# Kernel tuning notes

Hardware: AMD Instinct MI355X
Metric: run time of the kernel (lower is better)

The kernel has to match this reference:

```python
import jax, jax.numpy as jnp
import numpy as np

B, S, D_MODEL, D_SPACE = 4, 2048, 1024, 64
N = 512            # size of each neuron pool (all six equal)
TOTAL = 6 * N      # neuron_emb rows
K = 8              # top_k for all four attention branches
EPS = 1e-8


def topk_sparsify(w, k):
    """Top-k sparsification with renormalization via dense one-hot scatter-sum.
    w: [..., N] softmax probs -> sparse renormalized [..., N]."""
    vals, idx = jax.lax.top_k(w, k)                       # [..., k]
    n = w.shape[-1]
    one_hot = jax.nn.one_hot(idx, n, dtype=w.dtype)       # [..., k, N]
    sparse = (one_hot * vals[..., None]).sum(axis=-2)     # [..., N]
    return sparse / (sparse.sum(axis=-1, keepdims=True) + EPS)


def setup_inputs() -> dict:
    key = jax.random.key(0)
    kx, kw, ke = jax.random.split(key, 3)
    x = jax.random.normal(kx, (B, S, D_MODEL), dtype=jnp.float32)
    W_all = jax.random.normal(kw, (D_MODEL, 6 * D_SPACE), dtype=jnp.float32) * 0.02
    b_all = jnp.zeros((6 * D_SPACE,), dtype=jnp.float32)
    neuron_emb = jax.random.normal(ke, (TOTAL, D_SPACE), dtype=jnp.float32) * 0.02
    return {"x": x, "W_all": W_all, "b_all": b_all, "neuron_emb": neuron_emb}


def reference(x, W_all, b_all, neuron_emb):
    # L2-normalized neuron embeddings (cosine-sim logits)
    emb = neuron_emb / (jnp.linalg.norm(neuron_emb, axis=-1, keepdims=True) + EPS)
    # dense projection, then split into 6 heads of d_space (deterministic: no dropout)
    proj = x @ W_all + b_all                              # [B,S,6*d_space]
    h = jnp.split(proj, 6, axis=-1)
    # neuron_emb segments: fqk, fv, rqk, rv (knowledge segments unused here)
    segs = [emb[0:N], emb[0:N], emb[N:2 * N], emb[2 * N:3 * N], emb[2 * N:3 * N], emb[3 * N:4 * N]]
    weights = []
    for hi, ei in zip(h, segs):
        logits = jnp.einsum('bsd,nd->bsn', hi, ei)        # [B,S,N]
        pref = jax.nn.softmax(logits, axis=-1)
        weights.append(topk_sparsify(pref, K))
    # [6, B, S, N]: (fqk_Q, fqk_K, fv, rqk_Q, rqk_K, rv)
    return jnp.stack(weights, axis=0)
```

## Files before the change

kernel.cpp:

```cpp
#include <hip/hip_runtime.h>
#include <math.h>

#define NB 4
#define NS 2048
#define DMODEL 1024
#define DSPACE 64
#define NPOOL 512
#define NHEADS 6
#define NTOK (NB * NS)
#define PROJN (NHEADS * DSPACE)
#define EPSF 1e-8f

typedef float f32x2 __attribute__((ext_vector_type(2)));

#define PK_LO(ACC, A2, B2) \
    asm("v_pk_fma_f32 %0, %1, %2, %0 op_sel:[0,0,0] op_sel_hi:[1,0,1]" \
        : "+v"(ACC) : "v"(A2), "v"(B2))
#define PK_HI(ACC, A2, B2) \
    asm("v_pk_fma_f32 %0, %1, %2, %0 op_sel:[0,1,0] op_sel_hi:[1,1,1]" \
        : "+v"(ACC) : "v"(A2), "v"(B2))

__global__ __launch_bounds__(256) void k_norm_emb(const float* __restrict__ emb,
                                                  float* __restrict__ embT) {
    int row  = blockIdx.x * 4 + (threadIdx.x >> 6);
    int lane = threadIdx.x & 63;
    float v  = emb[row * DSPACE + lane];
    float ss = v * v;
#pragma unroll
    for (int off = 32; off >= 1; off >>= 1) ss += __shfl_xor(ss, off, 64);
    float nrm = sqrtf(ss) + EPSF;
    embT[lane * 2048 + row] = v / nrm;
}

__global__ __launch_bounds__(128, 4) void k_proj(const float* __restrict__ X,
                                                 const float* __restrict__ W,
                                                 const float* __restrict__ bias,
                                                 float* __restrict__ P, int KS) {
    __shared__ float Xt[16 * 128];
    __shared__ float Wt[2][16 * 64];
    const int tid = threadIdx.x;
    const int w   = tid >> 6;
    const int L   = tid & 63;
    const int bm  = blockIdx.x * 128;
    const int bn  = blockIdx.y * 64;
    const int z   = blockIdx.z;
    float* Pp = P + (size_t)z * NTOK * PROJN;

    const int r0  = (tid >> 3) << 2;
    const int c0  = (tid & 7) << 2;
    const int xrow = w * 32 + (L & 31) + ((L & 32) << 1);
    const int wrr = L >> 2;
    const int wcc = (L & 3) << 4;

    const float* Xrow = X + (size_t)(bm + xrow) * DMODEL;
    float* wtp = &Wt[w][0];

    f32x2 acc2[4][8];
#pragma unroll
    for (int p = 0; p < 4; ++p)
#pragma unroll
        for (int j = 0; j < 8; ++j) acc2[p][j] = (f32x2){0.f, 0.f};

    const int nsteps = KS >> 4;
    int k0 = z * KS;
    float4 xr0 = *(const float4*)&Xrow[k0 + 0];
    float4 xr1 = *(const float4*)&Xrow[k0 + 4];
    float4 xr2 = *(const float4*)&Xrow[k0 + 8];
    float4 xr3 = *(const float4*)&Xrow[k0 + 12];
    float4 wa0 = *(const float4*)&W[(size_t)(k0 + wrr) * PROJN + bn + wcc + 0];
    float4 wa1 = *(const float4*)&W[(size_t)(k0 + wrr) * PROJN + bn + wcc + 4];
    float4 wa2 = *(const float4*)&W[(size_t)(k0 + wrr) * PROJN + bn + wcc + 8];
    float4 wa3 = *(const float4*)&W[(size_t)(k0 + wrr) * PROJN + bn + wcc + 12];

    {
        Xt[ 0*128+xrow]=xr0.x; Xt[ 1*128+xrow]=xr0.y; Xt[ 2*128+xrow]=xr0.z; Xt[ 3*128+xrow]=xr0.w;
        Xt[ 4*128+xrow]=xr1.x; Xt[ 5*128+xrow]=xr1.y; Xt[ 6*128+xrow]=xr1.z; Xt[ 7*128+xrow]=xr1.w;
        Xt[ 8*128+xrow]=xr2.x; Xt[ 9*128+xrow]=xr2.y; Xt[10*128+xrow]=xr2.z; Xt[11*128+xrow]=xr2.w;
        Xt[12*128+xrow]=xr3.x; Xt[13*128+xrow]=xr3.y; Xt[14*128+xrow]=xr3.z; Xt[15*128+xrow]=xr3.w;
        *(float4*)&wtp[wrr * 64 + wcc + 0]  = wa0;
        *(float4*)&wtp[wrr * 64 + wcc + 4]  = wa1;
        *(float4*)&wtp[wrr * 64 + wcc + 8]  = wa2;
        *(float4*)&wtp[wrr * 64 + wcc + 12] = wa3;
    }

    for (int s = 0; s < nsteps; ++s) {
        if (s + 1 < nsteps) {
            int k1 = k0 + 16;
            xr0 = *(const float4*)&Xrow[k1 + 0];
            xr1 = *(const float4*)&Xrow[k1 + 4];
            xr2 = *(const float4*)&Xrow[k1 + 8];
            xr3 = *(const float4*)&Xrow[k1 + 12];
            wa0 = *(const float4*)&W[(size_t)(k1 + wrr) * PROJN + bn + wcc + 0];
            wa1 = *(const float4*)&W[(size_t)(k1 + wrr) * PROJN + bn + wcc + 4];
            wa2 = *(const float4*)&W[(size_t)(k1 + wrr) * PROJN + bn + wcc + 8];
            wa3 = *(const float4*)&W[(size_t)(k1 + wrr) * PROJN + bn + wcc + 12];
        }
#pragma unroll
        for (int kk = 0; kk < 16; ++kk) {
            float4 a0 = *(const float4*)&Xt[kk * 128 + r0];
            float4 a1 = *(const float4*)&Xt[kk * 128 + r0 + 64];
            float4 b0 = *(const float4*)&wtp[kk * 64 + c0];
            float4 b1 = *(const float4*)&wtp[kk * 64 + c0 + 32];
            f32x2 ap0 = (f32x2){a0.x, a0.y};
            f32x2 ap1 = (f32x2){a0.z, a0.w};
            f32x2 ap2 = (f32x2){a1.x, a1.y};
            f32x2 ap3 = (f32x2){a1.z, a1.w};
            f32x2 bq0 = (f32x2){b0.x, b0.y};
            f32x2 bq1 = (f32x2){b0.z, b0.w};
            f32x2 bq2 = (f32x2){b1.x, b1.y};
            f32x2 bq3 = (f32x2){b1.z, b1.w};
#pragma unroll
            for (int p = 0; p < 4; ++p) {
                f32x2 ap = (p == 0) ? ap0 : (p == 1) ? ap1 : (p == 2) ? ap2 : ap3;
                PK_LO(acc2[p][0], ap, bq0); PK_HI(acc2[p][1], ap, bq0);
                PK_LO(acc2[p][2], ap, bq1); PK_HI(acc2[p][3], ap, bq1);
                PK_LO(acc2[p][4], ap, bq2); PK_HI(acc2[p][5], ap, bq2);
                PK_LO(acc2[p][6], ap, bq3); PK_HI(acc2[p][7], ap, bq3);
            }
        }
        if (s + 1 < nsteps) {
            Xt[ 0*128+xrow]=xr0.x; Xt[ 1*128+xrow]=xr0.y; Xt[ 2*128+xrow]=xr0.z; Xt[ 3*128+xrow]=xr0.w;
            Xt[ 4*128+xrow]=xr1.x; Xt[ 5*128+xrow]=xr1.y; Xt[ 6*128+xrow]=xr1.z; Xt[ 7*128+xrow]=xr1.w;
            Xt[ 8*128+xrow]=xr2.x; Xt[ 9*128+xrow]=xr2.y; Xt[10*128+xrow]=xr2.z; Xt[11*128+xrow]=xr2.w;
            Xt[12*128+xrow]=xr3.x; Xt[13*128+xrow]=xr3.y; Xt[14*128+xrow]=xr3.z; Xt[15*128+xrow]=xr3.w;
            *(float4*)&wtp[wrr * 64 + wcc + 0]  = wa0;
            *(float4*)&wtp[wrr * 64 + wcc + 4]  = wa1;
            *(float4*)&wtp[wrr * 64 + wcc + 8]  = wa2;
            *(float4*)&wtp[wrr * 64 + wcc + 12] = wa3;
        }
        k0 += 16;
    }

#pragma unroll
    for (int i = 0; i < 8; ++i) {
        int row = bm + r0 + ((i < 4) ? i : 60 + i);
        float o0[4], o1[4];
#pragma unroll
        for (int j = 0; j < 4; ++j) {
            f32x2 v0 = acc2[i >> 1][j];
            f32x2 v1 = acc2[i >> 1][j + 4];
            o0[j] = (i & 1) ? v0.y : v0.x;
            o1[j] = (i & 1) ? v1.y : v1.x;
        }
        if (z == 0) {
#pragma unroll
            for (int j = 0; j < 4; ++j) {
                o0[j] += bias[bn + c0 + j];
                o1[j] += bias[bn + c0 + 32 + j];
            }
        }
        *(float4*)&Pp[(size_t)row * PROJN + bn + c0]      = *(float4*)&o0[0];
        *(float4*)&Pp[(size_t)row * PROJN + bn + c0 + 32] = *(float4*)&o1[0];
    }
}

#define CE(arr, a, b) { float _hi = fmaxf(arr[a], arr[b]); arr[b] = fminf(arr[a], arr[b]); arr[a] = _hi; }

#define SORT8(s) \
    CE(s,0,1) CE(s,2,3) CE(s,4,5) CE(s,6,7) \
    CE(s,0,2) CE(s,1,3) CE(s,4,6) CE(s,5,7) \
    CE(s,1,2) CE(s,5,6) \
    CE(s,0,4) CE(s,1,5) CE(s,2,6) CE(s,3,7) \
    CE(s,2,4) CE(s,3,5) \
    CE(s,1,2) CE(s,3,4) CE(s,5,6)

#define SWZ(v, IMM) __int_as_float(__builtin_amdgcn_ds_swizzle(__float_as_int(v), IMM))

#define BFLY_LEVEL(XCHG) { \
    float q[4][8]; \
    _Pragma("unroll") \
    for (int tt = 0; tt < 4; ++tt) { \
        _Pragma("unroll") \
        for (int i = 0; i < 8; ++i) { float _x = s[tt][i]; q[tt][i] = XCHG(_x); } \
    } \
    _Pragma("unroll") \
    for (int tt = 0; tt < 4; ++tt) { \
        float c[8]; \
        c[0] = fmaxf(s[tt][0], q[tt][7]); c[1] = fmaxf(s[tt][1], q[tt][6]); \
        c[2] = fmaxf(s[tt][2], q[tt][5]); c[3] = fmaxf(s[tt][3], q[tt][4]); \
        c[4] = fmaxf(s[tt][4], q[tt][3]); c[5] = fmaxf(s[tt][5], q[tt][2]); \
        c[6] = fmaxf(s[tt][6], q[tt][1]); c[7] = fmaxf(s[tt][7], q[tt][0]); \
        CE(c,0,4) CE(c,1,5) CE(c,2,6) CE(c,3,7) \
        CE(c,0,2) CE(c,1,3) CE(c,4,6) CE(c,5,7) \
        CE(c,0,1) CE(c,2,3) CE(c,4,5) CE(c,6,7) \
        _Pragma("unroll") \
        for (int i = 0; i < 8; ++i) s[tt][i] = c[i]; \
    } }

#define X1(v)  SWZ(v, 0x041F)
#define X2(v)  SWZ(v, 0x081F)
#define X4(v)  SWZ(v, 0x101F)
#define X8(v)  SWZ(v, 0x201F)
#define X16(v) SWZ(v, 0x401F)
#define X32(v) __shfl_xor(v, 32, 64)

__global__ __launch_bounds__(256, 2) void k_router(const float* __restrict__ P,
                                                   const float* __restrict__ embT,
                                                   float* __restrict__ out, int SK) {
    __shared__ float hsh[32][DSPACE];
    const int head = blockIdx.y;
    const int t0   = blockIdx.x * 32;
    const int tid  = threadIdx.x;
    const int wid  = tid >> 6;
    const int lane = tid & 63;
    const int so = (head == 2) ? 512 : (head == 3 || head == 4) ? 1024
                 : (head == 5) ? 1536 : 0;

    {
        int t  = (wid << 3) + (lane >> 3);
        int d0 = (lane & 7) << 3;
        size_t off = (size_t)(t0 + t) * PROJN + head * DSPACE + d0;
        float4 v0 = *(const float4*)&P[off];
        float4 v1 = *(const float4*)&P[off + 4];
        for (int ks = 1; ks < SK; ++ks) {
            size_t o2 = (size_t)ks * NTOK * PROJN + off;
            float4 u0 = *(const float4*)&P[o2];
            float4 u1 = *(const float4*)&P[o2 + 4];
            v0.x += u0.x; v0.y += u0.y; v0.z += u0.z; v0.w += u0.w;
            v1.x += u1.x; v1.y += u1.y; v1.z += u1.z; v1.w += u1.w;
        }
        *(float4*)&hsh[t][d0]     = v0;
        *(float4*)&hsh[t][d0 + 4] = v1;
    }

    f32x2 acc2[8][4];
#pragma unroll
    for (int t = 0; t < 8; ++t)
#pragma unroll
        for (int p = 0; p < 4; ++p) acc2[t][p] = (f32x2){0.f, 0.f};

    const float* ebase = &embT[so + (lane << 3)];
    for (int d4 = 0; d4 < DSPACE; d4 += 4) {
        f32x2 hp[8][2];
#pragma unroll
        for (int t = 0; t < 8; ++t) {
            hp[t][0] = *(const f32x2*)&hsh[(wid << 3) + t][d4];
            hp[t][1] = *(const f32x2*)&hsh[(wid << 3) + t][d4 + 2];
        }
#pragma unroll
        for (int dp = 0; dp < 2; ++dp) {
            const float* er0 = ebase + (size_t)(d4 + 2 * dp) * 2048;
            const float* er1 = er0 + 2048;
            f32x2 ea[4], eb[4];
#pragma unroll
            for (int p = 0; p < 4; ++p) {
                ea[p] = *(const f32x2*)&er0[2 * p];
                eb[p] = *(const f32x2*)&er1[2 * p];
            }
#pragma unroll
            for (int t = 0; t < 8; ++t) {
#pragma unroll
                for (int p = 0; p < 4; ++p) {
                    PK_LO(acc2[t][p], ea[p], hp[t][dp]);
                    PK_HI(acc2[t][p], eb[p], hp[t][dp]);
                }
            }
        }
    }

    const size_t obase = ((size_t)head * NTOK + t0 + (wid << 3)) * NPOOL;

#pragma unroll
    for (int g = 0; g < 2; ++g) {
        float l[4][8], s[4][8];
#pragma unroll
        for (int tt = 0; tt < 4; ++tt)
#pragma unroll
            for (int j = 0; j < 8; ++j) {
                f32x2 v = acc2[4 * g + tt][j >> 1];
                l[tt][j] = (j & 1) ? v.y : v.x;
                s[tt][j] = l[tt][j];
            }

        SORT8(s[0]) SORT8(s[1]) SORT8(s[2]) SORT8(s[3])

        BFLY_LEVEL(X1)
        BFLY_LEVEL(X2)
        BFLY_LEVEL(X4)
        BFLY_LEVEL(X8)
        BFLY_LEVEL(X16)
        BFLY_LEVEL(X32)

        unsigned gtm[4], eqm[4]; int own[4], inc[4];
#pragma unroll
        for (int tt = 0; tt < 4; ++tt) {
            const float T = s[tt][7];
            unsigned g_ = 0, e_ = 0; int cg = 0, ce = 0;
#pragma unroll
            for (int j = 0; j < 8; ++j) {
                if (l[tt][j] > T)       { g_ |= 1u << j; ++cg; }
                else if (l[tt][j] == T) { e_ |= 1u << j; ++ce; }
            }
            gtm[tt] = g_; eqm[tt] = e_;
            own[tt] = (ce << 8) | cg;
            inc[tt] = own[tt];
        }
#pragma unroll
        for (int off = 1; off < 64; off <<= 1) {
            int v0 = __shfl_up(inc[0], off, 64);
            int v1 = __shfl_up(inc[1], off, 64);
            int v2 = __shfl_up(inc[2], off, 64);
            int v3 = __shfl_up(inc[3], off, 64);
            if (lane >= off) { inc[0] += v0; inc[1] += v1; inc[2] += v2; inc[3] += v3; }
        }

#pragma unroll
        for (int tt = 0; tt < 4; ++tt) {
            const float T = s[tt][7];
            const float m = s[tt][0];
            int tot  = __shfl(inc[tt], 63, 64);
            int need = 8 - (tot & 0xff);
            int eqpre = (inc[tt] - own[tt]) >> 8;
            unsigned sel = gtm[tt];
#pragma unroll
            for (int j = 0; j < 8; ++j) {
                if ((eqm[tt] >> j) & 1u) { if (eqpre < need) sel |= 1u << j; ++eqpre; }
            }

            float s8 = 0.f;
#pragma unroll
            for (int i = 0; i < 8; ++i) s8 += __expf(s[tt][i] - m);
            float invd = 1.0f / s8;

            float o[8];
#pragma unroll
            for (int j = 0; j < 8; ++j)
                o[j] = ((sel >> j) & 1u) ? __expf(l[tt][j] - m) * invd : 0.0f;
            float4* dst = (float4*)&out[obase + (size_t)(4 * g + tt) * NPOOL + (lane << 3)];
            dst[0] = *(float4*)&o[0];
            dst[1] = *(float4*)&o[4];
        }
    }
}

extern "C" void kernel_launch(void* const* d_in, const int* in_sizes, int n_in,
                              void* d_out, int out_size, void* d_ws, size_t ws_size,
                              hipStream_t stream) {
    const float* x   = (const float*)d_in[0];
    const float* W   = (const float*)d_in[1];
    const float* b   = (const float*)d_in[2];
    const float* emb = (const float*)d_in[3];
    float* out  = (float*)d_out;
    float* embT = (float*)d_ws;
    float* proj = embT + 64 * 2048;

    size_t base = (size_t)64 * 2048 * 4;
    size_t slab = (size_t)NTOK * PROJN * 4;
    int SK = (ws_size >= base + 4 * slab) ? 4
           : (ws_size >= base + 2 * slab) ? 2 : 1;
    int KS = DMODEL / SK;

    k_norm_emb<<<dim3(512), dim3(256), 0, stream>>>(emb, embT);
    dim3 g2(NTOK / 128, PROJN / 64, SK);
    k_proj<<<g2, dim3(128), 0, stream>>>(x, W, b, proj, KS);
    dim3 g3(NTOK / 32, NHEADS);
    k_router<<<g3, dim3(256), 0, stream>>>(proj, embT, out, SK);
}
```

Before: 186.4 us.

## Drop LDS staging in projection GEMM, load X and W directly from global

The projection kernel no longer stages X and W tiles through shared memory with register double-buffering. Each thread now loads its own 8 X rows and 4 W rows per 4-wide k step straight from global memory (relying on L1/L2 caching) and accumulates with packed FMAs. This removes the LDS writes, reads and transposes, but makes the many threads that share X and W rows fetch them redundantly through the cache. Occupancy hints also change (k_proj min blocks 4→3, k_router 2→3), and an X4 macro is renamed to avoid clashing with the new X4 pointer.

```diff
diff --git a/kernel.cpp b/kernel.cpp
--- a/kernel.cpp
+++ b/kernel.cpp
@@ -12,6 +12,7 @@
 #define EPSF 1e-8f
 
 typedef float f32x2 __attribute__((ext_vector_type(2)));
+typedef float f32x4 __attribute__((ext_vector_type(4)));
 
 #define PK_LO(ACC, A2, B2) \
     asm("v_pk_fma_f32 %0, %1, %2, %0 op_sel:[0,0,0] op_sel_hi:[1,0,1]" \
@@ -20,6 +21,9 @@
     asm("v_pk_fma_f32 %0, %1, %2, %0 op_sel:[0,1,0] op_sel_hi:[1,1,1]" \
         : "+v"(ACC) : "v"(A2), "v"(B2))
 
+#define LO2(V4) __builtin_shufflevector(V4, V4, 0, 1)
+#define HI2(V4) __builtin_shufflevector(V4, V4, 2, 3)
+
 __global__ __launch_bounds__(256) void k_norm_emb(const float* __restrict__ emb,
                                                   float* __restrict__ embT) {
     int row  = blockIdx.x * 4 + (threadIdx.x >> 6);
@@ -32,116 +36,75 @@
     embT[lane * 2048 + row] = v / nrm;
 }
 
-__global__ __launch_bounds__(128, 4) void k_proj(const float* __restrict__ X,
+__global__ __launch_bounds__(128, 3) void k_proj(const float* __restrict__ X,
                                                  const float* __restrict__ W,
                                                  const float* __restrict__ bias,
                                                  float* __restrict__ P, int KS) {
-    __shared__ float Xt[16 * 128];
-    __shared__ float Wt[2][16 * 64];
     const int tid = threadIdx.x;
-    const int w   = tid >> 6;
-    const int L   = tid & 63;
     const int bm  = blockIdx.x * 128;
     const int bn  = blockIdx.y * 64;
     const int z   = blockIdx.z;
     float* Pp = P + (size_t)z * NTOK * PROJN;
 
-    const int r0  = (tid >> 3) << 2;
-    const int c0  = (tid & 7) << 2;
-    const int xrow = w * 32 + (L & 31) + ((L & 32) << 1);
-    const int wrr = L >> 2;
-    const int wcc = (L & 3) << 4;
-
-    const float* Xrow = X + (size_t)(bm + xrow) * DMODEL;
-    float* wtp = &Wt[w][0];
-
-    f32x2 acc2[4][8];
-#pragma unroll
-    for (int p = 0; p < 4; ++p)
-#pragma unroll
-        for (int j = 0; j < 8; ++j) acc2[p][j] = (f32x2){0.f, 0.f};
-
-    const int nsteps = KS >> 4;
-    int k0 = z * KS;
-    float4 xr0 = *(const float4*)&Xrow[k0 + 0];
-    float4 xr1 = *(const float4*)&Xrow[k0 + 4];
-    float4 xr2 = *(const float4*)&Xrow[k0 + 8];
-    float4 xr3 = *(const float4*)&Xrow[k0 + 12];
-    float4 wa0 = *(const float4*)&W[(size_t)(k0 + wrr) * PROJN + bn + wcc + 0];
-    float4 wa1 = *(const float4*)&W[(size_t)(k0 + wrr) * PROJN + bn + wcc + 4];
-    float4 wa2 = *(const float4*)&W[(size_t)(k0 + wrr) * PROJN + bn + wcc + 8];
-    float4 wa3 = *(const float4*)&W[(size_t)(k0 + wrr) * PROJN + bn + wcc + 12];
-
-    {
-        Xt[ 0*128+xrow]=xr0.x; Xt[ 1*128+xrow]=xr0.y; Xt[ 2*128+xrow]=xr0.z; Xt[ 3*128+xrow]=xr0.w;
-        Xt[ 4*128+xrow]=xr1.x; Xt[ 5*128+xrow]=xr1.y; Xt[ 6*128+xrow]=xr1.z; Xt[ 7*128+xrow]=xr1.w;
-        Xt[ 8*128+xrow]=xr2.x; Xt[ 9*128+xrow]=xr2.y; Xt[10*128+xrow]=xr2.z; Xt[11*128+xrow]=xr2.w;
-        Xt[12*128+xrow]=xr3.x; Xt[13*128+xrow]=xr3.y; Xt[14*128+xrow]=xr3.z; Xt[15*128+xrow]=xr3.w;
-        *(float4*)&wtp[wrr * 64 + wcc + 0]  = wa0;
-        *(float4*)&wtp[wrr * 64 + wcc + 4]  = wa1;
-        *(float4*)&wtp[wrr * 64 + wcc + 8]  = wa2;
-        *(float4*)&wtp[wrr * 64 + wcc + 12] = wa3;
-    }
-
-    for (int s = 0; s < nsteps; ++s) {
-        if (s + 1 < nsteps) {
-            int k1 = k0 + 16;
-            xr0 = *(const float4*)&Xrow[k1 + 0];
-            xr1 = *(const float4*)&Xrow[k1 + 4];
-            xr2 = *(const float4*)&Xrow[k1 + 8];
-            xr3 = *(const float4*)&Xrow[k1 + 12];
-            wa0 = *(const float4*)&W[(size_t)(k1 + wrr) * PROJN + bn + wcc + 0];
-            wa1 = *(const float4*)&W[(size_t)(k1 + wrr) * PROJN + bn + wcc + 4];
-            wa2 = *(const float4*)&W[(size_t)(k1 + wrr) * PROJN + bn + wcc + 8];
-            wa3 = *(const float4*)&W[(size_t)(k1 + wrr) * PROJN + bn + wcc + 12];
-        }
-#pragma unroll
-        for (int kk = 0; kk < 16; ++kk) {
-            float4 a0 = *(const float4*)&Xt[kk * 128 + r0];
-            float4 a1 = *(const float4*)&Xt[kk * 128 + r0 + 64];
-            float4 b0 = *(const float4*)&wtp[kk * 64 + c0];
-            float4 b1 = *(const float4*)&wtp[kk * 64 + c0 + 32];
-            f32x2 ap0 = (f32x2){a0.x, a0.y};
-            f32x2 ap1 = (f32x2){a0.z, a0.w};
-            f32x2 ap2 = (f32x2){a1.x, a1.y};
-            f32x2 ap3 = (f32x2){a1.z, a1.w};
-            f32x2 bq0 = (f32x2){b0.x, b0.y};
-            f32x2 bq1 = (f32x2){b0.z, b0.w};
-            f32x2 bq2 = (f32x2){b1.x, b1.y};
-            f32x2 bq3 = (f32x2){b1.z, b1.w};
-#pragma unroll
-            for (int p = 0; p < 4; ++p) {
-                f32x2 ap = (p == 0) ? ap0 : (p == 1) ? ap1 : (p == 2) ? ap2 : ap3;
-                PK_LO(acc2[p][0], ap, bq0); PK_HI(acc2[p][1], ap, bq0);
-                PK_LO(acc2[p][2], ap, bq1); PK_HI(acc2[p][3], ap, bq1);
-                PK_LO(acc2[p][4], ap, bq2); PK_HI(acc2[p][5], ap, bq2);
-                PK_LO(acc2[p][6], ap, bq3); PK_HI(acc2[p][7], ap, bq3);
-            }
-        }
-        if (s + 1 < nsteps) {
-            Xt[ 0*128+xrow]=xr0.x; Xt[ 1*128+xrow]=xr0.y; Xt[ 2*128+xrow]=xr0.z; Xt[ 3*128+xrow]=xr0.w;
-            Xt[ 4*128+xrow]=xr1.x; Xt[ 5*128+xrow]=xr1.y; Xt[ 6*128+xrow]=xr1.z; Xt[ 7*128+xrow]=xr1.w;
-            Xt[ 8*128+xrow]=xr2.x; Xt[ 9*128+xrow]=xr2.y; Xt[10*128+xrow]=xr2.z; Xt[11*128+xrow]=xr2.w;
-            Xt[12*128+xrow]=xr3.x; Xt[13*128+xrow]=xr3.y; Xt[14*128+xrow]=xr3.z; Xt[15*128+xrow]=xr3.w;
-            *(float4*)&wtp[wrr * 64 + wcc + 0]  = wa0;
-            *(float4*)&wtp[wrr * 64 + wcc + 4]  = wa1;
-            *(float4*)&wtp[wrr * 64 + wcc + 8]  = wa2;
-            *(float4*)&wtp[wrr * 64 + wcc + 12] = wa3;
-        }
-        k0 += 16;
+    const int r0 = (tid >> 3) << 2;
+    const int c0 = (tid & 7) << 2;
+
+    const float* X0 = X + (size_t)(bm + r0) * DMODEL;
+    const float* X4 = X + (size_t)(bm + r0 + 64) * DMODEL;
+
+    f32x2 acc2[8][4];
+#pragma unroll
+    for (int i = 0; i < 8; ++i)
+#pragma unroll
+        for (int jp = 0; jp < 4; ++jp) acc2[i][jp] = (f32x2){0.f, 0.f};
+
+    const int k0 = z * KS;
+    for (int g = 0; g < KS; g += 4) {
+        const int kb = k0 + g;
+        f32x4 xr[8];
+#pragma unroll
+        for (int i = 0; i < 4; ++i) {
+            xr[i]     = *(const f32x4*)&X0[(size_t)i * DMODEL + kb];
+            xr[i + 4] = *(const f32x4*)&X4[(size_t)i * DMODEL + kb];
+        }
+        f32x4 wq[4][2];
+#pragma unroll
+        for (int q = 0; q < 4; ++q) {
+            const float* wrow = &W[(size_t)(kb + q) * PROJN + bn];
+            wq[q][0] = *(const f32x4*)&wrow[c0];
+            wq[q][1] = *(const f32x4*)&wrow[c0 + 32];
+        }
+#pragma unroll
+        for (int i = 0; i < 8; ++i) {
+            f32x2 xlo = LO2(xr[i]);
+            f32x2 xhi = HI2(xr[i]);
+            PK_LO(acc2[i][0], LO2(wq[0][0]), xlo);
+            PK_LO(acc2[i][1], HI2(wq[0][0]), xlo);
+            PK_LO(acc2[i][2], LO2(wq[0][1]), xlo);
+            PK_LO(acc2[i][3], HI2(wq[0][1]), xlo);
+            PK_HI(acc2[i][0], LO2(wq[1][0]), xlo);
+            PK_HI(acc2[i][1], HI2(wq[1][0]), xlo);
+            PK_HI(acc2[i][2], LO2(wq[1][1]), xlo);
+            PK_HI(acc2[i][3], HI2(wq[1][1]), xlo);
+            PK_LO(acc2[i][0], LO2(wq[2][0]), xhi);
+            PK_LO(acc2[i][1], HI2(wq[2][0]), xhi);
+            PK_LO(acc2[i][2], LO2(wq[2][1]), xhi);
+            PK_LO(acc2[i][3], HI2(wq[2][1]), xhi);
+            PK_HI(acc2[i][0], LO2(wq[3][0]), xhi);
+            PK_HI(acc2[i][1], HI2(wq[3][0]), xhi);
+            PK_HI(acc2[i][2], LO2(wq[3][1]), xhi);
+            PK_HI(acc2[i][3], HI2(wq[3][1]), xhi);
+        }
     }
 
 #pragma unroll
     for (int i = 0; i < 8; ++i) {
         int row = bm + r0 + ((i < 4) ? i : 60 + i);
         float o0[4], o1[4];
-#pragma unroll
-        for (int j = 0; j < 4; ++j) {
-            f32x2 v0 = acc2[i >> 1][j];
-            f32x2 v1 = acc2[i >> 1][j + 4];
-            o0[j] = (i & 1) ? v0.y : v0.x;
-            o1[j] = (i & 1) ? v1.y : v1.x;
-        }
+        o0[0] = acc2[i][0].x; o0[1] = acc2[i][0].y;
+        o0[2] = acc2[i][1].x; o0[3] = acc2[i][1].y;
+        o1[0] = acc2[i][2].x; o1[1] = acc2[i][2].y;
+        o1[2] = acc2[i][3].x; o1[3] = acc2[i][3].y;
         if (z == 0) {
 #pragma unroll
             for (int j = 0; j < 4; ++j) {
@@ -189,12 +152,12 @@
 
 #define X1(v)  SWZ(v, 0x041F)
 #define X2(v)  SWZ(v, 0x081F)
-#define X4(v)  SWZ(v, 0x101F)
+#define X4_(v) SWZ(v, 0x101F)
 #define X8(v)  SWZ(v, 0x201F)
 #define X16(v) SWZ(v, 0x401F)
 #define X32(v) __shfl_xor(v, 32, 64)
 
-__global__ __launch_bounds__(256, 2) void k_router(const float* __restrict__ P,
+__global__ __launch_bounds__(256, 3) void k_router(const float* __restrict__ P,
                                                    const float* __restrict__ embT,
                                                    float* __restrict__ out, int SK) {
     __shared__ float hsh[32][DSPACE];
@@ -276,7 +239,7 @@
 
         BFLY_LEVEL(X1)
         BFLY_LEVEL(X2)
-        BFLY_LEVEL(X4)
+        BFLY_LEVEL(X4_)
         BFLY_LEVEL(X8)
         BFLY_LEVEL(X16)
         BFLY_LEVEL(X32)
```

After: 207.3 us. +11.2%, slower.
